# Kernel tuning notes

Measured on AMD Instinct MI355X. Metric: run time of the kernel, lower is better.

## Reference

```python
import jax, jax.numpy as jnp
import numpy as np

T, D, E, DFF, TOPK, CAP = 4096, 1024, 16, 1024, 2, 512


def setup_inputs() -> dict:
    key = jax.random.key(0)
    k1, k2, k3, k4 = jax.random.split(key, 4)
    h = jax.random.normal(k1, (T, D), jnp.float32)
    Wr = jax.random.normal(k2, (D, E), jnp.float32) / np.sqrt(D).astype(np.float32)
    W1 = jax.random.normal(k3, (E, D, DFF), jnp.float32) / np.sqrt(D).astype(np.float32)
    W2 = jax.random.normal(k4, (E, DFF, D), jnp.float32) / np.sqrt(DFF).astype(np.float32)
    return {"h": h, "Wr": Wr, "W1": W1, "W2": W2, "topk": TOPK, "capacity": CAP}


def reference(h, Wr, W1, W2, topk, capacity):
    # One routing hop of DNA: top-k router -> capacity_selection -> grouped
    # (vmapped) expert execution -> weighted combine with residual rescale.
    Tn, Dn = h.shape
    En = Wr.shape[1]
    C = min(int(capacity), Tn)

    # --- Router: linear logits, softmax probs, top-k expert mask per token ---
    logits = h @ Wr                                  # [T, E]
    probs = jax.nn.softmax(logits, axis=-1)          # [T, E]
    _, tk_idx = jax.lax.top_k(logits, int(topk))     # [T, topk]
    mask_te = jnp.zeros((Tn, En), bool).at[jnp.arange(Tn)[:, None], tk_idx].set(True)

    # --- capacity_selection (gather form of the one-hot slot einsum) ---
    mask_et = mask_te.T                              # [E, T]
    score_et = jnp.where(mask_et, logits.T, -jnp.inf)
    _, top_indices = jax.lax.top_k(score_et, C)      # [E, C] token ids per slot
    valid = jnp.take_along_axis(mask_et, top_indices, axis=1)  # [E, C] slot active
    e_idx = jnp.arange(En)[:, None]
    kept = (jnp.zeros((En, Tn), jnp.int32)
            .at[e_idx, top_indices].add(valid.astype(jnp.int32)) > 0)  # [E, T]

    # --- sort active slots by original token position (stable) ---
    pos = jnp.where(valid, top_indices, Tn + 1)
    order = jnp.argsort(pos, axis=1, stable=True)
    top_sorted = jnp.take_along_axis(top_indices, order, axis=1)     # [E, C]
    valid_sorted = jnp.take_along_axis(valid, order, axis=1)         # [E, C]

    # --- dispatch: equivalent to einsum('ect,td->ecd', slot, h) ---
    xin = h[top_sorted] * valid_sorted[..., None]    # [E, C, d]

    # --- grouped expert execution (vmap over stacked params via einsum) ---
    hidden = jax.nn.gelu(jnp.einsum('ecd,edf->ecf', xin, W1))
    expert_out = jnp.einsum('ecf,efd->ecd', hidden, W2)             # [E, C, d]

    # --- combine: weights = routing probs masked by capacity-kept tokens ---
    combine_w = jnp.where(kept.T, probs, 0.0)        # [T, E]
    rho = combine_w.sum(axis=1, keepdims=True)       # [T, 1]
    w_ec = jnp.take_along_axis(combine_w.T, top_sorted, axis=1) * valid_sorted  # [E, C]
    combine = (jnp.zeros((Tn, Dn), h.dtype)
               .at[top_sorted.reshape(-1)]
               .add((expert_out * w_ec[..., None]).reshape(-1, Dn)))
    return h + combine - rho * h
```

## Files before the change

kernel.cpp:

```cpp
#include <hip/hip_runtime.h>
#include <hip/hip_bf16.h>
#include <stdint.h>

#define T_TOK 4096
#define DIM   1024
#define NE    16
#define NDFF  1024
#define CAPN  512

typedef unsigned int   u32;
typedef unsigned short u16;
typedef __attribute__((ext_vector_type(8))) short bf16x8;
typedef __attribute__((ext_vector_type(4))) float f32x4;

__device__ __forceinline__ void gll16(void* lds, const void* g) {
  union { const void* p; const __attribute__((address_space(1))) void* q; } gu;
  union { void* p; __attribute__((address_space(3))) void* q; } lu;
  gu.p = g; lu.p = lds;
  __builtin_amdgcn_global_load_lds(gu.q, lu.q, 16, 0, 0);
}

__device__ __forceinline__ u16 f2bf(float f) {
  u32 u = __float_as_uint(f);
  u32 r = (u + 0x7FFFu + ((u >> 16) & 1u)) >> 16;
  return (u16)r;
}

__device__ __forceinline__ float gelu_tanh(float x) {
  float x3 = x * x * x;
  float z = 0.7978845608028654f * (x + 0.044715f * x3);
  float t = __expf(2.0f * z);
  float th = 1.0f - 2.0f / (t + 1.0f);
  return 0.5f * x * (1.0f + th);
}

__global__ __launch_bounds__(256) void router_kernel(
    const float* __restrict__ h, const float* __restrict__ Wr,
    float* __restrict__ logits, u32* __restrict__ topmask, u32* __restrict__ keptmask)
{
  const int t = blockIdx.x * 4 + (threadIdx.x >> 6);
  const int lane = threadIdx.x & 63;
  float acc[NE];
#pragma unroll
  for (int e = 0; e < NE; ++e) acc[e] = 0.f;
  const float* hrow = h + (size_t)t * DIM;
#pragma unroll 4
  for (int i = 0; i < DIM / 64; ++i) {
    int d = lane + 64 * i;
    float hv = hrow[d];
    const float4* wr4 = (const float4*)(Wr + (size_t)d * NE);
#pragma unroll
    for (int q = 0; q < 4; ++q) {
      float4 w = wr4[q];
      acc[q*4+0] += hv * w.x; acc[q*4+1] += hv * w.y;
      acc[q*4+2] += hv * w.z; acc[q*4+3] += hv * w.w;
    }
  }
#pragma unroll
  for (int e = 0; e < NE; ++e) {
    float v = acc[e];
#pragma unroll
    for (int off = 32; off; off >>= 1) v += __shfl_xor(v, off);
    acc[e] = v;
  }
  int m1 = 0; float b1 = acc[0];
#pragma unroll
  for (int e = 1; e < NE; ++e) if (acc[e] > b1) { b1 = acc[e]; m1 = e; }
  int m2 = 0; float b2 = -3.4e38f;
#pragma unroll
  for (int e = 0; e < NE; ++e) if (e != m1 && acc[e] > b2) { b2 = acc[e]; m2 = e; }
  if (lane < NE) logits[(size_t)t * NE + lane] = acc[lane];
  if (lane == 0) { topmask[t] = (1u << m1) | (1u << m2); keptmask[t] = 0u; }
}

__global__ __launch_bounds__(1024) void capacity_kernel(
    const float* __restrict__ logits, const u32* __restrict__ topmask,
    u32* __restrict__ keptmask, int* __restrict__ expert_tokens)
{
  const int e = blockIdx.x;
  const int tid = threadIdx.x;
  const int lane = tid & 63, wv = tid >> 6;
  __shared__ u32 wred[16];
  __shared__ u32 wscan[16];
  __shared__ u32 bcast;

  u32 key[4];
#pragma unroll
  for (int j = 0; j < 4; ++j) {
    int t = tid * 4 + j;
    float lg = logits[(size_t)t * NE + e];
    u32 u = __float_as_uint(lg);
    u32 ord = (u >> 31) ? ~u : (u | 0x80000000u);
    bool sel = (topmask[t] >> e) & 1u;
    key[j] = sel ? ord : 0u;
  }

  auto blockReduce = [&](u32 v) -> u32 {
#pragma unroll
    for (int off = 32; off; off >>= 1) v += __shfl_xor(v, off);
    if (lane == 0) wred[wv] = v;
    __syncthreads();
    if (tid == 0) { u32 s = 0; for (int i = 0; i < 16; ++i) s += wred[i]; bcast = s; }
    __syncthreads();
    u32 r = bcast;
    __syncthreads();
    return r;
  };

  u32 nsel = blockReduce((key[0] != 0u) + (key[1] != 0u) + (key[2] != 0u) + (key[3] != 0u));

  u32 p = 0, need = 0;
  if (nsel > CAPN) {
    need = CAPN;
    for (int b = 31; b >= 0; --b) {
      u32 cand = p | (1u << b);
      u32 hi = ~((1u << b) - 1u);
      u32 loc = 0;
#pragma unroll
      for (int j = 0; j < 4; ++j) loc += ((key[j] & hi) == cand) ? 1u : 0u;
      u32 c = blockReduce(loc);
      if (c >= need) p = cand; else need -= c;
    }
  }

  auto blockExScan = [&](u32 v, u32& total) -> u32 {
    u32 x = v;
#pragma unroll
    for (int off = 1; off < 64; off <<= 1) { u32 y = __shfl_up(x, off); if (lane >= off) x += y; }
    if (lane == 63) wscan[wv] = x;
    __syncthreads();
    if (wv == 0) {
      u32 w = (lane < 16) ? wscan[lane] : 0u;
#pragma unroll
      for (int off = 1; off < 16; off <<= 1) { u32 y = __shfl_up(w, off); if (lane >= off) w += y; }
      if (lane < 16) wscan[lane] = w;
    }
    __syncthreads();
    u32 base = wv ? wscan[wv - 1] : 0u;
    total = wscan[15];
    __syncthreads();
    return base + x - v;
  };

  bool eq[4], kept[4];
  u32 eqc = 0;
#pragma unroll
  for (int j = 0; j < 4; ++j) { eq[j] = (key[j] != 0u) && (key[j] == p); eqc += eq[j] ? 1u : 0u; }
  u32 eqtot;
  u32 eqbase = blockExScan(eqc, eqtot);
  u32 keptc = 0;
  {
    u32 er = eqbase;
#pragma unroll
    for (int j = 0; j < 4; ++j) {
      kept[j] = (key[j] != 0u) && ((key[j] > p) || (eq[j] && er < need));
      er += eq[j] ? 1u : 0u;
      keptc += kept[j] ? 1u : 0u;
    }
  }
  u32 ktot;
  u32 kbase = blockExScan(keptc, ktot);
  {
    u32 slot = kbase;
#pragma unroll
    for (int j = 0; j < 4; ++j) {
      if (kept[j]) {
        int t = tid * 4 + j;
        expert_tokens[e * CAPN + slot] = t;
        atomicOr(&keptmask[t], 1u << e);
        slot++;
      }
    }
  }
  for (u32 i = ktot + tid; i < CAPN; i += 1024) expert_tokens[e * CAPN + i] = -1;
}

__global__ __launch_bounds__(256) void rho_init_kernel(
    const float* __restrict__ h, const float* __restrict__ logits,
    const u32* __restrict__ keptmask, float* __restrict__ out)
{
  const int t = blockIdx.x * 4 + (threadIdx.x >> 6);
  const int lane = threadIdx.x & 63;
  float v[NE]; float m = -3.4e38f;
#pragma unroll
  for (int i = 0; i < NE; ++i) { v[i] = logits[(size_t)t * NE + i]; m = fmaxf(m, v[i]); }
  float sum = 0.f;
#pragma unroll
  for (int i = 0; i < NE; ++i) { v[i] = expf(v[i] - m); sum += v[i]; }
  u32 km = keptmask[t];
  float rho = 0.f;
#pragma unroll
  for (int i = 0; i < NE; ++i) if ((km >> i) & 1u) rho += v[i];
  rho /= sum;
  float s = 1.0f - rho;
  const float4* hp4 = (const float4*)(h + (size_t)t * DIM);
  float4* op4 = (float4*)(out + (size_t)t * DIM);
#pragma unroll
  for (int i = 0; i < 4; ++i) {
    const float4 hv = hp4[lane + 64 * i];
    float4 o; o.x = hv.x * s; o.y = hv.y * s; o.z = hv.z * s; o.w = hv.w * s;
    op4[lane + 64 * i] = o;
  }
}

__global__ __launch_bounds__(256) void gather_kernel(
    const float* __restrict__ h, const int* __restrict__ expert_tokens,
    const float* __restrict__ logits, u16* __restrict__ Xg, float* __restrict__ w_ec)
{
  const int slot = blockIdx.x * 4 + (threadIdx.x >> 6);
  const int lane = threadIdx.x & 63;
  const int t = expert_tokens[slot];
  u16* dst = Xg + (size_t)slot * DIM + lane * 16;
  if (t < 0) {
    if (lane == 0) w_ec[slot] = 0.f;
    uint4 z = make_uint4(0, 0, 0, 0);
    *(uint4*)dst = z; *(uint4*)(dst + 8) = z;
  } else {
    if (lane == 0) {
      const int e = slot / CAPN;
      float v[NE], m = -3.4e38f;
#pragma unroll
      for (int i = 0; i < NE; ++i) { v[i] = logits[(size_t)t * NE + i]; m = fmaxf(m, v[i]); }
      float sum = 0.f;
#pragma unroll
      for (int i = 0; i < NE; ++i) { v[i] = expf(v[i] - m); sum += v[i]; }
      w_ec[slot] = v[e] / sum;
    }
    const float4* src = (const float4*)(h + (size_t)t * DIM + lane * 16);
    __align__(16) u16 tmp[16];
#pragma unroll
    for (int q = 0; q < 4; ++q) {
      float4 x = src[q];
      tmp[q*4+0] = f2bf(x.x); tmp[q*4+1] = f2bf(x.y);
      tmp[q*4+2] = f2bf(x.z); tmp[q*4+3] = f2bf(x.w);
    }
    *(uint4*)dst = *(const uint4*)tmp;
    *(uint4*)(dst + 8) = *(const uint4*)(tmp + 8);
  }
}

#define LDS_TOTAL 98304

template <int EPI>
__global__ __launch_bounds__(512) void gemm_fused_kernel(
    const u16* __restrict__ Abase, const float* __restrict__ Bf32base,
    u16* __restrict__ Hout, float* __restrict__ out,
    const int* __restrict__ expert_tokens, const float* __restrict__ w_ec)
{
  extern __shared__ __align__(16) char smem[];
  char* As = smem;
  char* Bs = smem + 65536;

  const int p   = blockIdx.x + 8 * (blockIdx.y + 2 * blockIdx.z);
  const int lin = (p & 7) * 32 + (p >> 3);
  const int e   = lin >> 4;
  const int rem = lin & 15;
  const int m0  = (rem >> 3) * 256;
  const int n0  = (rem & 7) * 128;

  const char*  A = (const char*)(Abase + (size_t)e * 512 * 1024);
  const float* B = Bf32base + (size_t)e * 1024 * 1024;

  const int tid = threadIdx.x;
  const int lane = tid & 63, wave = tid >> 6;
  const int wr = wave >> 1, wc = wave & 1;
  f32x4 acc[4][4];
#pragma unroll
  for (int i = 0; i < 4; ++i)
#pragma unroll
    for (int j = 0; j < 4; ++j) acc[i][j] = (f32x4){0.f, 0.f, 0.f, 0.f};

  const int srow  = lane >> 3;
  const int sbyte = 16 * ((lane & 7) ^ srow);
  const u32 asBase = (u32)(uintptr_t)As;
  const u32 bsTr0 = (u32)(uintptr_t)Bs + (u32)((lane >> 4) * 128 + (lane & 15) * 8);

  auto stageA = [&](int kt, int buf) {
    const int kb0 = kt * 128;
#pragma unroll
    for (int i = 0; i < 4; ++i) {
      const int c = wave * 4 + i;
      const int r = c * 8 + srow;
      gll16(As + buf * 32768 + c * 1024, A + (size_t)(m0 + r) * 2048 + kb0 + sbyte);
    }
  };
  auto loadB = [&](float4* br, int kt) {
    const int k0 = kt * 64;
#pragma unroll
    for (int it = 0; it < 2; ++it) {
      const int q = tid + 512 * it;
      const int kl = q >> 4, n8 = q & 15;
      const float* gp = B + (size_t)(k0 + kl) * 1024 + n0 + n8 * 8;
      br[2*it]   = *(const float4*)gp;
      br[2*it+1] = *(const float4*)(gp + 4);
    }
  };
  auto writeB = [&](const float4* br, int buf) {
#pragma unroll
    for (int it = 0; it < 2; ++it) {
      const int q = tid + 512 * it;
      const int kl = q >> 4, n8 = q & 15;
      const int c = (n8 >> 1) * 2 + ((kl >> 2) & 1);
      const int byt = c * 1024 + (kl >> 3) * 128 + (kl & 3) * 32 + (n8 & 1) * 16;
      const float* f = (const float*)&br[2*it];
      u32 d[4];
#pragma unroll
      for (int j = 0; j < 4; ++j) {
        __hip_bfloat162 pk = __float22bfloat162_rn(make_float2(f[2*j], f[2*j+1]));
        d[j] = *(const u32*)&pk;
      }
      *(uint4*)(Bs + buf * 16384 + byt) = *(const uint4*)d;
    }
  };
  auto compute = [&](int buf) {
#pragma unroll
    for (int s = 0; s < 2; ++s) {
      const int kb = (s * 64 + (lane >> 4) * 16) ^ ((lane & 7) << 4);
      bf16x8 af[4];
      unsigned long long tlo[4], thi[4];
#pragma unroll
      for (int i = 0; i < 4; ++i) {
        const int rowa = wr * 64 + i * 16 + (lane & 15);
        const u32 aaddr = asBase + (u32)(buf * 32768 + rowa * 128 + kb);
        asm volatile("ds_read_b128 %0, %1" : "=v"(af[i]) : "v"(aaddr) : "memory");
      }
#pragma unroll
      for (int j = 0; j < 4; ++j) {
        const u32 a = bsTr0 + (u32)(buf * 16384 + (wc * 4 + j) * 2048 + s * 512);
        asm volatile("ds_read_b64_tr_b16 %0, %2 offset:0\n\t"
                     "ds_read_b64_tr_b16 %1, %2 offset:1024"
                     : "=v"(tlo[j]), "=v"(thi[j]) : "v"(a) : "memory");
      }
#pragma unroll
      for (int j = 0; j < 4; ++j) {
        if (j == 0)      asm volatile("s_waitcnt lgkmcnt(6)" ::: "memory");
        else if (j == 1) asm volatile("s_waitcnt lgkmcnt(4)" ::: "memory");
        else if (j == 2) asm volatile("s_waitcnt lgkmcnt(2)" ::: "memory");
        else             asm volatile("s_waitcnt lgkmcnt(0)" ::: "memory");
        __builtin_amdgcn_sched_barrier(0);
        union { unsigned long long q[2]; bf16x8 v; } u;
        u.q[0] = tlo[j]; u.q[1] = thi[j];
        const bf16x8 bfv = u.v;
#pragma unroll
        for (int i = 0; i < 4; ++i)
          acc[i][j] = __builtin_amdgcn_mfma_f32_16x16x32_bf16(af[i], bfv, acc[i][j], 0, 0, 0);
      }
    }
  };

  stageA(0, 0);
  {
    float4 br0[4];
    loadB(br0, 0);
    writeB(br0, 0);
  }
  float4 brE[4], brO[4];
  loadB(brO, 1);
  __syncthreads();

  for (int kt = 0; kt < 16; kt += 2) {
    if (kt + 2 < 16) loadB(brE, kt + 2);
    if (kt + 1 < 16) stageA(kt + 1, 1);
    compute(0);
    if (kt + 1 < 16) writeB(brO, 1);
    __syncthreads();
    if (kt + 1 < 16) {
      if (kt + 3 < 16) loadB(brO, kt + 3);
      if (kt + 2 < 16) stageA(kt + 2, 0);
      compute(1);
      if (kt + 2 < 16) writeB(brE, 0);
      __syncthreads();
    }
  }

  if (EPI == 1) {
#pragma unroll
    for (int i = 0; i < 4; ++i) {
#pragma unroll
      for (int r = 0; r < 4; ++r) {
        const int row = m0 + wr * 64 + i * 16 + (lane >> 4) * 4 + r;
        u16* hp = Hout + ((size_t)e * 512 + row) * 1024 + n0 + wc * 64 + (lane & 15);
#pragma unroll
        for (int j = 0; j < 4; ++j) hp[j * 16] = f2bf(gelu_tanh(acc[i][j][r]));
      }
    }
  } else {
#pragma unroll
    for (int i = 0; i < 4; ++i) {
#pragma unroll
      for (int r = 0; r < 4; ++r) {
        const int row  = m0 + wr * 64 + i * 16 + (lane >> 4) * 4 + r;
        const int slot = e * CAPN + row;
        const int t = expert_tokens[slot];
        if (t >= 0) {
          const float w = w_ec[slot];
          float* op = out + (size_t)t * DIM + n0 + wc * 64 + (lane & 15);
#pragma unroll
          for (int j = 0; j < 4; ++j) atomicAdd(op + j * 16, acc[i][j][r] * w);
        }
      }
    }
  }
}

extern "C" void kernel_launch(void* const* d_in, const int* in_sizes, int n_in,
                              void* d_out, int out_size, void* d_ws, size_t ws_size,
                              hipStream_t stream)
{
  const float* h  = (const float*)d_in[0];
  const float* Wr = (const float*)d_in[1];
  const float* W1 = (const float*)d_in[2];
  const float* W2 = (const float*)d_in[3];
  float* out = (float*)d_out;

  char* ws = (char*)d_ws;
  u16* Xg  = (u16*)(ws);
  u16* Hb  = (u16*)(ws + 16777216);
  float* logits       = (float*)(ws + 33554432);
  u32*   topmask      = (u32*)  (ws + 33816576);
  u32*   keptmask     = (u32*)  (ws + 33832960);
  int*   expert_tokens= (int*)  (ws + 33849344);
  float* w_ec         = (float*)(ws + 33882112);

  (void)hipFuncSetAttribute(reinterpret_cast<const void*>(&gemm_fused_kernel<1>),
                            hipFuncAttributeMaxDynamicSharedMemorySize, LDS_TOTAL);
  (void)hipFuncSetAttribute(reinterpret_cast<const void*>(&gemm_fused_kernel<2>),
                            hipFuncAttributeMaxDynamicSharedMemorySize, LDS_TOTAL);

  router_kernel<<<T_TOK / 4, 256, 0, stream>>>(h, Wr, logits, topmask, keptmask);
  capacity_kernel<<<NE, 1024, 0, stream>>>(logits, topmask, keptmask, expert_tokens);
  rho_init_kernel<<<T_TOK / 4, 256, 0, stream>>>(h, logits, keptmask, out);
  gather_kernel<<<NE * CAPN / 4, 256, 0, stream>>>(h, expert_tokens, logits, Xg, w_ec);
  gemm_fused_kernel<1><<<dim3(8, 2, NE), 512, LDS_TOTAL, stream>>>(Xg, W1, Hb, nullptr, nullptr, nullptr);
  gemm_fused_kernel<2><<<dim3(8, 2, NE), 512, LDS_TOTAL, stream>>>(Hb, W2, nullptr, out, expert_tokens, w_ec);
}
```

Measured before the change: 137.2 us.

## Retile expert GEMMs to full 512-row M by 64-col N blocks

```diff
diff --git a/kernel.cpp b/kernel.cpp
--- a/kernel.cpp
+++ b/kernel.cpp
@@ -239,7 +239,7 @@
   }
 }
 
-#define LDS_TOTAL 98304
+#define LDS_TOTAL 147456
 
 template <int EPI>
 __global__ __launch_bounds__(512) void gemm_fused_kernel(
@@ -249,21 +249,19 @@
 {
   extern __shared__ __align__(16) char smem[];
   char* As = smem;
-  char* Bs = smem + 65536;
-
-  const int p   = blockIdx.x + 8 * (blockIdx.y + 2 * blockIdx.z);
+  char* Bs = smem + 131072;
+
+  const int p   = blockIdx.x + 16 * blockIdx.z;
   const int lin = (p & 7) * 32 + (p >> 3);
   const int e   = lin >> 4;
   const int rem = lin & 15;
-  const int m0  = (rem >> 3) * 256;
-  const int n0  = (rem & 7) * 128;
+  const int n0  = rem * 64;
 
   const char*  A = (const char*)(Abase + (size_t)e * 512 * 1024);
   const float* B = Bf32base + (size_t)e * 1024 * 1024;
 
   const int tid = threadIdx.x;
   const int lane = tid & 63, wave = tid >> 6;
-  const int wr = wave >> 1, wc = wave & 1;
   f32x4 acc[4][4];
 #pragma unroll
   for (int i = 0; i < 4; ++i)
@@ -278,39 +276,31 @@
   auto stageA = [&](int kt, int buf) {
     const int kb0 = kt * 128;
 #pragma unroll
-    for (int i = 0; i < 4; ++i) {
-      const int c = wave * 4 + i;
+    for (int i = 0; i < 8; ++i) {
+      const int c = wave * 8 + i;
       const int r = c * 8 + srow;
-      gll16(As + buf * 32768 + c * 1024, A + (size_t)(m0 + r) * 2048 + kb0 + sbyte);
+      gll16(As + buf * 65536 + c * 1024, A + (size_t)r * 2048 + kb0 + sbyte);
     }
   };
   auto loadB = [&](float4* br, int kt) {
     const int k0 = kt * 64;
-#pragma unroll
-    for (int it = 0; it < 2; ++it) {
-      const int q = tid + 512 * it;
-      const int kl = q >> 4, n8 = q & 15;
-      const float* gp = B + (size_t)(k0 + kl) * 1024 + n0 + n8 * 8;
-      br[2*it]   = *(const float4*)gp;
-      br[2*it+1] = *(const float4*)(gp + 4);
-    }
+    const int kl = tid >> 3, n8 = tid & 7;
+    const float* gp = B + (size_t)(k0 + kl) * 1024 + n0 + n8 * 8;
+    br[0] = *(const float4*)gp;
+    br[1] = *(const float4*)(gp + 4);
   };
   auto writeB = [&](const float4* br, int buf) {
-#pragma unroll
-    for (int it = 0; it < 2; ++it) {
-      const int q = tid + 512 * it;
-      const int kl = q >> 4, n8 = q & 15;
-      const int c = (n8 >> 1) * 2 + ((kl >> 2) & 1);
-      const int byt = c * 1024 + (kl >> 3) * 128 + (kl & 3) * 32 + (n8 & 1) * 16;
-      const float* f = (const float*)&br[2*it];
-      u32 d[4];
-#pragma unroll
-      for (int j = 0; j < 4; ++j) {
-        __hip_bfloat162 pk = __float22bfloat162_rn(make_float2(f[2*j], f[2*j+1]));
-        d[j] = *(const u32*)&pk;
-      }
-      *(uint4*)(Bs + buf * 16384 + byt) = *(const uint4*)d;
-    }
+    const int kl = tid >> 3, n8 = tid & 7;
+    const int c = (n8 >> 1) * 2 + ((kl >> 2) & 1);
+    const int byt = c * 1024 + (kl >> 3) * 128 + (kl & 3) * 32 + (n8 & 1) * 16;
+    const float* f = (const float*)br;
+    u32 d[4];
+#pragma unroll
+    for (int j = 0; j < 4; ++j) {
+      __hip_bfloat162 pk = __float22bfloat162_rn(make_float2(f[2*j], f[2*j+1]));
+      d[j] = *(const u32*)&pk;
+    }
+    *(uint4*)(Bs + buf * 8192 + byt) = *(const uint4*)d;
   };
   auto compute = [&](int buf) {
 #pragma unroll
@@ -320,13 +310,13 @@
       unsigned long long tlo[4], thi[4];
 #pragma unroll
       for (int i = 0; i < 4; ++i) {
-        const int rowa = wr * 64 + i * 16 + (lane & 15);
-        const u32 aaddr = asBase + (u32)(buf * 32768 + rowa * 128 + kb);
+        const int rowa = wave * 64 + i * 16 + (lane & 15);
+        const u32 aaddr = asBase + (u32)(buf * 65536 + rowa * 128 + kb);
         asm volatile("ds_read_b128 %0, %1" : "=v"(af[i]) : "v"(aaddr) : "memory");
       }
 #pragma unroll
       for (int j = 0; j < 4; ++j) {
-        const u32 a = bsTr0 + (u32)(buf * 16384 + (wc * 4 + j) * 2048 + s * 512);
+        const u32 a = bsTr0 + (u32)(buf * 8192 + j * 2048 + s * 512);
         asm volatile("ds_read_b64_tr_b16 %0, %2 offset:0\n\t"
                      "ds_read_b64_tr_b16 %1, %2 offset:1024"
                      : "=v"(tlo[j]), "=v"(thi[j]) : "v"(a) : "memory");
@@ -350,11 +340,11 @@
 
   stageA(0, 0);
   {
-    float4 br0[4];
+    float4 br0[2];
     loadB(br0, 0);
     writeB(br0, 0);
   }
-  float4 brE[4], brO[4];
+  float4 brE[2], brO[2];
   loadB(brO, 1);
   __syncthreads();
 
@@ -378,8 +368,8 @@
     for (int i = 0; i < 4; ++i) {
 #pragma unroll
       for (int r = 0; r < 4; ++r) {
-        const int row = m0 + wr * 64 + i * 16 + (lane >> 4) * 4 + r;
-        u16* hp = Hout + ((size_t)e * 512 + row) * 1024 + n0 + wc * 64 + (lane & 15);
+        const int row = wave * 64 + i * 16 + (lane >> 4) * 4 + r;
+        u16* hp = Hout + ((size_t)e * 512 + row) * 1024 + n0 + (lane & 15);
 #pragma unroll
         for (int j = 0; j < 4; ++j) hp[j * 16] = f2bf(gelu_tanh(acc[i][j][r]));
       }
@@ -389,12 +379,12 @@
     for (int i = 0; i < 4; ++i) {
 #pragma unroll
       for (int r = 0; r < 4; ++r) {
-        const int row  = m0 + wr * 64 + i * 16 + (lane >> 4) * 4 + r;
+        const int row  = wave * 64 + i * 16 + (lane >> 4) * 4 + r;
         const int slot = e * CAPN + row;
         const int t = expert_tokens[slot];
         if (t >= 0) {
           const float w = w_ec[slot];
-          float* op = out + (size_t)t * DIM + n0 + wc * 64 + (lane & 15);
+          float* op = out + (size_t)t * DIM + n0 + (lane & 15);
 #pragma unroll
           for (int j = 0; j < 4; ++j) atomicAdd(op + j * 16, acc[i][j][r] * w);
         }
@@ -431,6 +421,6 @@
   capacity_kernel<<<NE, 1024, 0, stream>>>(logits, topmask, keptmask, expert_tokens);
   rho_init_kernel<<<T_TOK / 4, 256, 0, stream>>>(h, logits, keptmask, out);
   gather_kernel<<<NE * CAPN / 4, 256, 0, stream>>>(h, expert_tokens, logits, Xg, w_ec);
-  gemm_fused_kernel<1><<<dim3(8, 2, NE), 512, LDS_TOTAL, stream>>>(Xg, W1, Hb, nullptr, nullptr, nullptr);
-  gemm_fused_kernel<2><<<dim3(8, 2, NE), 512, LDS_TOTAL, stream>>>(Hb, W2, nullptr, out, expert_tokens, w_ec);
-}
+  gemm_fused_kernel<1><<<dim3(16, 1, NE), 512, LDS_TOTAL, stream>>>(Xg, W1, Hb, nullptr, nullptr, nullptr);
+  gemm_fused_kernel<2><<<dim3(16, 1, NE), 512, LDS_TOTAL, stream>>>(Hb, W2, nullptr, out, expert_tokens, w_ec);
+}
```

New measurement: 142.2 us. 3.7% more time.
